# Kernel tuning notes

Measured on AMD Instinct MI355X. Metric: run time of the kernel, lower is better.

The kernel has to match this reference:

```python
import jax, jax.numpy as jnp
import numpy as np
import math

# Hardcoded model constants (from source globals)
N_LAYERS = 4
MAX_SEQ_LEN = 34
VOCAB_SIZE = 14
TOK_DIM = 3
POS_DIM = 3
D_MODEL = 6
HEAD_DIM = 3
N_POS = 10
MAX_DIGITS = 10
ANSWER_LEN = 11
X_START, PLUS_POS, Y_START, EQ_POS, Z_START, EOS_POS = 0, 10, 11, 21, 22, 33
PLUS_TOKEN, EQUALS_TOKEN, EOS_TOKEN, PAD_TOKEN = 10, 11, 12, 13
BATCH = 16384


def _spiral(i, p):
    return (math.cos(2 * math.pi * i / p), math.sin(2 * math.pi * i / p), i / max(p - 1, 1))


def _build_pos_enc():
    pe = np.zeros((MAX_SEQ_LEN, POS_DIM), np.float32)
    for i in range(MAX_DIGITS):
        pe[X_START + i] = _spiral(i, N_POS)
    for i in range(MAX_DIGITS):
        pe[Y_START + i] = _spiral(i, N_POS)
    for i in range(min(ANSWER_LEN, N_POS)):
        pe[Z_START + i] = _spiral(i, N_POS)
    pe[Z_START + 10] = [0.0, 0.0, 1.5]
    pe[PLUS_POS] = [2.0, 0.0, -1.0]
    pe[EQ_POS] = [0.0, 2.0, -1.0]
    pe[EOS_POS] = [-2.0, 0.0, -1.0]
    return jnp.asarray(pe)


def _build_tok_emb():
    emb = np.zeros((VOCAB_SIZE, TOK_DIM), np.float32)
    for d in range(10):
        emb[d] = _spiral(d, 10)
    emb[PLUS_TOKEN] = [2.0, 0.0, -1.0]
    emb[EQUALS_TOKEN] = [0.0, 2.0, -1.0]
    emb[EOS_TOKEN] = [-2.0, 0.0, -1.0]
    emb[PAD_TOKEN] = [0.0, -2.0, -1.0]
    return jnp.asarray(emb)


def _xavier(key, shape):
    fan_out, fan_in = shape[-2], shape[-1]
    bound = math.sqrt(6.0 / (fan_in + fan_out))
    return jax.random.uniform(key, shape, jnp.float32, -bound, bound)


def setup_inputs() -> dict:
    key = jax.random.key(0)
    ks = jax.random.split(key, 10)
    L = N_LAYERS
    return {
        "idx": jax.random.randint(ks[0], (BATCH, MAX_SEQ_LEN), 0, VOCAB_SIZE),
        "tok_emb": _build_tok_emb(),
        "pos_enc": _build_pos_enc(),
        "ln_w": jnp.ones((L, D_MODEL), jnp.float32),
        "ln_b": jnp.zeros((L, D_MODEL), jnp.float32),
        "q1w": _xavier(ks[1], (L, HEAD_DIM, TOK_DIM)),
        "k1w": _xavier(ks[2], (L, HEAD_DIM, TOK_DIM)),
        "v1w": _xavier(ks[3], (L, HEAD_DIM, TOK_DIM)),
        "q2w": _xavier(ks[4], (L, HEAD_DIM, POS_DIM)),
        "k2w": _xavier(ks[5], (L, HEAD_DIM, POS_DIM)),
        "v2w": _xavier(ks[6], (L, HEAD_DIM, POS_DIM)),
        "out_w": _xavier(ks[7], (L, D_MODEL, 2 * HEAD_DIM)),
        "lnf_w": jnp.ones((D_MODEL,), jnp.float32),
        "lnf_b": jnp.zeros((D_MODEL,), jnp.float32),
        "head_w": _xavier(ks[8], (VOCAB_SIZE, D_MODEL)),
    }


def _layernorm(x, w, b, eps=1e-5):
    m = jnp.mean(x, -1, keepdims=True)
    v = jnp.mean(jnp.square(x - m), -1, keepdims=True)
    return (x - m) * jax.lax.rsqrt(v + eps) * w + b


def _attend(q, k, v, mask):
    # q,k,v: [B,T,HEAD_DIM]; mask: [T,T] bool lower-triangular
    s = jnp.einsum('bqd,bkd->bqk', q, k) / math.sqrt(HEAD_DIM)
    s = jnp.where(mask, s, jnp.finfo(s.dtype).min)
    return jnp.einsum('bqk,bkd->bqd', jax.nn.softmax(s, axis=-1), v)


def reference(idx, tok_emb, pos_enc, ln_w, ln_b, q1w, k1w, v1w, q2w, k2w, v2w, out_w, lnf_w, lnf_b, head_w):
    B, T = idx.shape
    tok = tok_emb[idx]                                   # [B,T,3]
    pos = jnp.broadcast_to(pos_enc[:T], (B, T, POS_DIM))  # [B,T,3]
    x = jnp.concatenate([tok, pos], axis=-1)             # [B,T,6]
    mask = jnp.tril(jnp.ones((T, T), bool))
    for l in range(N_LAYERS):
        h = _layernorm(x, ln_w[l], ln_b[l])
        ht, hp = h[..., :TOK_DIM], h[..., TOK_DIM:]
        o1 = _attend(ht @ q1w[l].T, ht @ k1w[l].T, ht @ v1w[l].T, mask)
        o2 = _attend(hp @ q2w[l].T, hp @ k2w[l].T, hp @ v2w[l].T, mask)
        x = x + jnp.concatenate([o1, o2], axis=-1) @ out_w[l].T
    x = _layernorm(x, lnf_w, lnf_b)
    return x @ head_w.T                                  # [B,T,VOCAB]
```

## Files before the change

kernel.cpp:

```cpp
#include <hip/hip_runtime.h>
#include <math.h>

#define N_LAYERS 4
#define SEQ      34
#define BATCH_N  16384
#define NE       16
#define NSLOT    16
#define NT       3
#define VOCAB    14
#define QSCALE   0.8329806647638704f

__global__ __launch_bounds__(NE * NSLOT) void addtrans_kernel(
    const int*   __restrict__ idx,
    const float* __restrict__ tok_emb,
    const float* __restrict__ pos_enc,
    const float* __restrict__ ln_w,
    const float* __restrict__ ln_b,
    const float* __restrict__ q1w,
    const float* __restrict__ k1w,
    const float* __restrict__ v1w,
    const float* __restrict__ q2w,
    const float* __restrict__ k2w,
    const float* __restrict__ v2w,
    const float* __restrict__ out_w,
    const float* __restrict__ lnf_w,
    const float* __restrict__ lnf_b,
    const float* __restrict__ head_w,
    float* __restrict__ out)
{
    __shared__ float4 kvs[3 * SEQ + 1][NE];

    const int x = threadIdx.x & (NE - 1);
    const int y = threadIdx.x >> 4;
    const int b = (int)blockIdx.x * NE + x;

    int tp[NT];
    tp[0] = 33 - y;
    tp[1] = y;
    tp[2] = (y == 15) ? 16 : ((y == 14) ? 17 : -1);
    const int jmax = tp[0];

    float xs[NT][6];
    #pragma unroll
    for (int k = 0; k < NT; ++k) {
        const int t = tp[k];
        if (t >= 0) {
            const int tok = idx[(size_t)b * SEQ + t];
            xs[k][0] = tok_emb[tok * 3 + 0];
            xs[k][1] = tok_emb[tok * 3 + 1];
            xs[k][2] = tok_emb[tok * 3 + 2];
            xs[k][3] = pos_enc[t * 3 + 0];
            xs[k][4] = pos_enc[t * 3 + 1];
            xs[k][5] = pos_enc[t * 3 + 2];
        }
    }

    float qs[NT][6];

    for (int l = 0; l < N_LAYERS; ++l) {
        __syncthreads();

        #pragma unroll
        for (int k = 0; k < NT; ++k) {
            const int t = tp[k];
            if (t >= 0) {
                float h[6];
                {
                    const float* v = xs[k];
                    float m = (v[0]+v[1]+v[2]+v[3]+v[4]+v[5]) * (1.0f/6.0f);
                    float var = 0.f;
                    #pragma unroll
                    for (int i = 0; i < 6; ++i) { float d = v[i]-m; var += d*d; }
                    var *= (1.0f/6.0f);
                    float r = rsqrtf(var + 1e-5f);
                    #pragma unroll
                    for (int i = 0; i < 6; ++i)
                        h[i] = (v[i]-m) * r * ln_w[l*6+i] + ln_b[l*6+i];
                }
                float kk[6], vv[6];
                #pragma unroll
                for (int i = 0; i < 3; ++i) {
                    const int w = l*9 + i*3;
                    qs[k][i]   = (q1w[w]*h[0] + q1w[w+1]*h[1] + q1w[w+2]*h[2]) * QSCALE;
                    kk[i]      =  k1w[w]*h[0] + k1w[w+1]*h[1] + k1w[w+2]*h[2];
                    vv[i]      =  v1w[w]*h[0] + v1w[w+1]*h[1] + v1w[w+2]*h[2];
                    qs[k][3+i] = (q2w[w]*h[3] + q2w[w+1]*h[4] + q2w[w+2]*h[5]) * QSCALE;
                    kk[3+i]    =  k2w[w]*h[3] + k2w[w+1]*h[4] + k2w[w+2]*h[5];
                    vv[3+i]    =  v2w[w]*h[3] + v2w[w+1]*h[4] + v2w[w+2]*h[5];
                }
                kvs[0*SEQ + t][x] = make_float4(kk[0], kk[1], kk[2], kk[3]);
                kvs[1*SEQ + t][x] = make_float4(kk[4], kk[5], vv[0], vv[1]);
                kvs[2*SEQ + t][x] = make_float4(vv[2], vv[3], vv[4], vv[5]);
            }
        }
        __syncthreads();

        float l1[NT], l2[NT], a[NT][6];
        #pragma unroll
        for (int k = 0; k < NT; ++k) {
            l1[k] = 0.f; l2[k] = 0.f;
            #pragma unroll
            for (int i = 0; i < 6; ++i) a[k][i] = 0.f;
        }
        float4 c0 = kvs[0][x], c1 = kvs[SEQ][x], c2 = kvs[2*SEQ][x];
        #pragma unroll 2
        for (int j = 0; j <= jmax; ++j) {
            float4 n0 = kvs[j + 1][x];
            float4 n1 = kvs[SEQ + j + 1][x];
            float4 n2 = kvs[2*SEQ + j + 1][x];
            #pragma unroll
            for (int k = 0; k < NT; ++k) {
                if (k == 0 || j <= tp[k]) {
                    float s1 = qs[k][0]*c0.x + qs[k][1]*c0.y + qs[k][2]*c0.z;
                    float s2 = qs[k][3]*c0.w + qs[k][4]*c1.x + qs[k][5]*c1.y;
                    float p1 = __builtin_amdgcn_exp2f(s1);
                    float p2 = __builtin_amdgcn_exp2f(s2);
                    l1[k] += p1;        l2[k] += p2;
                    a[k][0] += p1*c1.z; a[k][1] += p1*c1.w; a[k][2] += p1*c2.x;
                    a[k][3] += p2*c2.y; a[k][4] += p2*c2.z; a[k][5] += p2*c2.w;
                }
            }
            c0 = n0; c1 = n1; c2 = n2;
        }

        #pragma unroll
        for (int k = 0; k < NT; ++k) {
            if (tp[k] >= 0) {
                const float i1 = __builtin_amdgcn_rcpf(l1[k]);
                const float i2 = __builtin_amdgcn_rcpf(l2[k]);
                float o[6] = { a[k][0]*i1, a[k][1]*i1, a[k][2]*i1,
                               a[k][3]*i2, a[k][4]*i2, a[k][5]*i2 };
                #pragma unroll
                for (int i = 0; i < 6; ++i) {
                    const int w = l*36 + i*6;
                    xs[k][i] += out_w[w+0]*o[0] + out_w[w+1]*o[1] + out_w[w+2]*o[2]
                              + out_w[w+3]*o[3] + out_w[w+4]*o[4] + out_w[w+5]*o[5];
                }
            }
        }
    }

    #pragma unroll
    for (int k = 0; k < NT; ++k) {
        const int t = tp[k];
        if (t >= 0) {
            float hf[6];
            {
                const float* v = xs[k];
                float m = (v[0]+v[1]+v[2]+v[3]+v[4]+v[5]) * (1.0f/6.0f);
                float var = 0.f;
                #pragma unroll
                for (int i = 0; i < 6; ++i) { float d = v[i]-m; var += d*d; }
                var *= (1.0f/6.0f);
                float r = rsqrtf(var + 1e-5f);
                #pragma unroll
                for (int i = 0; i < 6; ++i)
                    hf[i] = (v[i]-m) * r * lnf_w[i] + lnf_b[i];
            }
            float lg[VOCAB];
            #pragma unroll
            for (int c = 0; c < VOCAB; ++c) {
                const int w = c*6;
                lg[c] = head_w[w+0]*hf[0] + head_w[w+1]*hf[1] + head_w[w+2]*hf[2]
                      + head_w[w+3]*hf[3] + head_w[w+4]*hf[4] + head_w[w+5]*hf[5];
            }
            float2* op = (float2*)(out + ((size_t)b * SEQ + t) * VOCAB);
            #pragma unroll
            for (int c = 0; c < 7; ++c)
                op[c] = make_float2(lg[2*c], lg[2*c+1]);
        }
    }
}

extern "C" void kernel_launch(void* const* d_in, const int* in_sizes, int n_in,
                              void* d_out, int out_size, void* d_ws, size_t ws_size,
                              hipStream_t stream) {
    const int*   idx     = (const int*)  d_in[0];
    const float* tok_emb = (const float*)d_in[1];
    const float* pos_enc = (const float*)d_in[2];
    const float* ln_w    = (const float*)d_in[3];
    const float* ln_b    = (const float*)d_in[4];
    const float* q1w     = (const float*)d_in[5];
    const float* k1w     = (const float*)d_in[6];
    const float* v1w     = (const float*)d_in[7];
    const float* q2w     = (const float*)d_in[8];
    const float* k2w     = (const float*)d_in[9];
    const float* v2w     = (const float*)d_in[10];
    const float* out_w   = (const float*)d_in[11];
    const float* lnf_w   = (const float*)d_in[12];
    const float* lnf_b   = (const float*)d_in[13];
    const float* head_w  = (const float*)d_in[14];
    float* out = (float*)d_out;

    const int grid = BATCH_N / NE;
    addtrans_kernel<<<grid, NE * NSLOT, 0, stream>>>(
        idx, tok_emb, pos_enc, ln_w, ln_b,
        q1w, k1w, v1w, q2w, k2w, v2w,
        out_w, lnf_w, lnf_b, head_w, out);
}
```

Measured before the change: 153.1 us.

## Reassign query rows to 8 slots with strided mapping and packed float2 math

Blocks shrink from 256 to 128 threads, and each thread now owns up to five query rows spaced eight apart instead of a balanced pair of rows. The key loop is split into phases so that rows drop out as the causal range ends, which removes the per-row predicate. The two attention heads are interleaved in float2 vectors so the compiler can emit packed FP32 FMAs. The cost is more registers per thread and smaller blocks, which may reduce occupancy and change load balance across threads.

```diff
diff --git a/kernel.cpp b/kernel.cpp
--- a/kernel.cpp
+++ b/kernel.cpp
@@ -5,10 +5,16 @@
 #define SEQ      34
 #define BATCH_N  16384
 #define NE       16
-#define NSLOT    16
-#define NT       3
+#define NSLOT    8
+#define NT       5
 #define VOCAB    14
 #define QSCALE   0.8329806647638704f
+
+typedef float f32x2 __attribute__((ext_vector_type(2)));
+
+static __device__ __forceinline__ f32x2 mk2(float a, float b) {
+    f32x2 r; r.x = a; r.y = b; return r;
+}
 
 __global__ __launch_bounds__(NE * NSLOT) void addtrans_kernel(
     const int*   __restrict__ idx,
@@ -34,16 +40,17 @@
     const int y = threadIdx.x >> 4;
     const int b = (int)blockIdx.x * NE + x;
 
-    int tp[NT];
-    tp[0] = 33 - y;
-    tp[1] = y;
-    tp[2] = (y == 15) ? 16 : ((y == 14) ? 17 : -1);
-    const int jmax = tp[0];
+    int rp[NT];
+    rp[0] = y;
+    rp[1] = 8 + y;
+    rp[2] = 16 + y;
+    rp[3] = 24 + y;
+    rp[4] = (y < 2) ? (32 + y) : -1;
 
     float xs[NT][6];
     #pragma unroll
     for (int k = 0; k < NT; ++k) {
-        const int t = tp[k];
+        const int t = rp[k];
         if (t >= 0) {
             const int tok = idx[(size_t)b * SEQ + t];
             xs[k][0] = tok_emb[tok * 3 + 0];
@@ -55,14 +62,16 @@
         }
     }
 
-    float qs[NT][6];
+    f32x2 qp[NT][3];
+    #pragma unroll
+    for (int i = 0; i < 3; ++i) qp[4][i] = mk2(0.f, 0.f);
 
     for (int l = 0; l < N_LAYERS; ++l) {
         __syncthreads();
 
         #pragma unroll
         for (int k = 0; k < NT; ++k) {
-            const int t = tp[k];
+            const int t = rp[k];
             if (t >= 0) {
                 float h[6];
                 {
@@ -77,64 +86,82 @@
                     for (int i = 0; i < 6; ++i)
                         h[i] = (v[i]-m) * r * ln_w[l*6+i] + ln_b[l*6+i];
                 }
-                float kk[6], vv[6];
+                f32x2 hp0 = mk2(h[0], h[3]);
+                f32x2 hp1 = mk2(h[1], h[4]);
+                f32x2 hp2 = mk2(h[2], h[5]);
+                f32x2 kkp[3], vvp[3];
                 #pragma unroll
                 for (int i = 0; i < 3; ++i) {
                     const int w = l*9 + i*3;
-                    qs[k][i]   = (q1w[w]*h[0] + q1w[w+1]*h[1] + q1w[w+2]*h[2]) * QSCALE;
-                    kk[i]      =  k1w[w]*h[0] + k1w[w+1]*h[1] + k1w[w+2]*h[2];
-                    vv[i]      =  v1w[w]*h[0] + v1w[w+1]*h[1] + v1w[w+2]*h[2];
-                    qs[k][3+i] = (q2w[w]*h[3] + q2w[w+1]*h[4] + q2w[w+2]*h[5]) * QSCALE;
-                    kk[3+i]    =  k2w[w]*h[3] + k2w[w+1]*h[4] + k2w[w+2]*h[5];
-                    vv[3+i]    =  v2w[w]*h[3] + v2w[w+1]*h[4] + v2w[w+2]*h[5];
+                    f32x2 q = mk2(q1w[w  ], q2w[w  ]) * hp0
+                            + mk2(q1w[w+1], q2w[w+1]) * hp1
+                            + mk2(q1w[w+2], q2w[w+2]) * hp2;
+                    qp[k][i] = q * QSCALE;
+                    kkp[i]   = mk2(k1w[w  ], k2w[w  ]) * hp0
+                             + mk2(k1w[w+1], k2w[w+1]) * hp1
+                             + mk2(k1w[w+2], k2w[w+2]) * hp2;
+                    vvp[i]   = mk2(v1w[w  ], v2w[w  ]) * hp0
+                             + mk2(v1w[w+1], v2w[w+1]) * hp1
+                             + mk2(v1w[w+2], v2w[w+2]) * hp2;
                 }
-                kvs[0*SEQ + t][x] = make_float4(kk[0], kk[1], kk[2], kk[3]);
-                kvs[1*SEQ + t][x] = make_float4(kk[4], kk[5], vv[0], vv[1]);
-                kvs[2*SEQ + t][x] = make_float4(vv[2], vv[3], vv[4], vv[5]);
+                kvs[0*SEQ + t][x] = make_float4(kkp[0].x, kkp[0].y, kkp[1].x, kkp[1].y);
+                kvs[1*SEQ + t][x] = make_float4(kkp[2].x, kkp[2].y, vvp[0].x, vvp[0].y);
+                kvs[2*SEQ + t][x] = make_float4(vvp[1].x, vvp[1].y, vvp[2].x, vvp[2].y);
             }
         }
         __syncthreads();
 
-        float l1[NT], l2[NT], a[NT][6];
+        f32x2 ls[NT], acc[NT][3];
         #pragma unroll
         for (int k = 0; k < NT; ++k) {
-            l1[k] = 0.f; l2[k] = 0.f;
-            #pragma unroll
-            for (int i = 0; i < 6; ++i) a[k][i] = 0.f;
-        }
+            ls[k] = mk2(0.f, 0.f);
+            acc[k][0] = acc[k][1] = acc[k][2] = mk2(0.f, 0.f);
+        }
+
         float4 c0 = kvs[0][x], c1 = kvs[SEQ][x], c2 = kvs[2*SEQ][x];
-        #pragma unroll 2
-        for (int j = 0; j <= jmax; ++j) {
-            float4 n0 = kvs[j + 1][x];
-            float4 n1 = kvs[SEQ + j + 1][x];
-            float4 n2 = kvs[2*SEQ + j + 1][x];
-            #pragma unroll
-            for (int k = 0; k < NT; ++k) {
-                if (k == 0 || j <= tp[k]) {
-                    float s1 = qs[k][0]*c0.x + qs[k][1]*c0.y + qs[k][2]*c0.z;
-                    float s2 = qs[k][3]*c0.w + qs[k][4]*c1.x + qs[k][5]*c1.y;
-                    float p1 = __builtin_amdgcn_exp2f(s1);
-                    float p2 = __builtin_amdgcn_exp2f(s2);
-                    l1[k] += p1;        l2[k] += p2;
-                    a[k][0] += p1*c1.z; a[k][1] += p1*c1.w; a[k][2] += p1*c2.x;
-                    a[k][3] += p2*c2.y; a[k][4] += p2*c2.z; a[k][5] += p2*c2.w;
-                }
-            }
-            c0 = n0; c1 = n1; c2 = n2;
-        }
+        int j = 0;
+
+        #define LOADN \
+            float4 n0 = kvs[j + 1][x]; \
+            float4 n1 = kvs[SEQ + j + 1][x]; \
+            float4 n2 = kvs[2*SEQ + j + 1][x]; \
+            f32x2 kp0 = mk2(c0.x, c0.y), kp1 = mk2(c0.z, c0.w), kp2 = mk2(c1.x, c1.y); \
+            f32x2 vp0 = mk2(c1.z, c1.w), vp1 = mk2(c2.x, c2.y), vp2 = mk2(c2.z, c2.w);
+        #define ROWM(k) { \
+            f32x2 s = qp[k][0]*kp0 + qp[k][1]*kp1 + qp[k][2]*kp2; \
+            f32x2 p = mk2(__builtin_amdgcn_exp2f(s.x), __builtin_amdgcn_exp2f(s.y)); \
+            ls[k] += p; \
+            acc[k][0] += p*vp0; acc[k][1] += p*vp1; acc[k][2] += p*vp2; }
+        #define ROLL c0 = n0; c1 = n1; c2 = n2;
+
+        for (; j <= rp[0]; ++j) { LOADN ROWM(0) ROWM(1) ROWM(2) ROWM(3) ROWM(4) ROLL }
+        #pragma unroll
+        for (int it = 0; it < 8; ++it, ++j) { LOADN ROWM(1) ROWM(2) ROWM(3) ROWM(4) ROLL }
+        #pragma unroll
+        for (int it = 0; it < 8; ++it, ++j) { LOADN ROWM(2) ROWM(3) ROWM(4) ROLL }
+        #pragma unroll
+        for (int it = 0; it < 8; ++it, ++j) { LOADN ROWM(3) ROWM(4) ROLL }
+        for (; j <= rp[4]; ++j) { LOADN ROWM(4) ROLL }
+
+        #undef LOADN
+        #undef ROWM
+        #undef ROLL
 
         #pragma unroll
         for (int k = 0; k < NT; ++k) {
-            if (tp[k] >= 0) {
-                const float i1 = __builtin_amdgcn_rcpf(l1[k]);
-                const float i2 = __builtin_amdgcn_rcpf(l2[k]);
-                float o[6] = { a[k][0]*i1, a[k][1]*i1, a[k][2]*i1,
-                               a[k][3]*i2, a[k][4]*i2, a[k][5]*i2 };
+            if (rp[k] >= 0) {
+                const f32x2 inv = mk2(__builtin_amdgcn_rcpf(ls[k].x),
+                                      __builtin_amdgcn_rcpf(ls[k].y));
+                f32x2 op0 = acc[k][0] * inv;
+                f32x2 op1 = acc[k][1] * inv;
+                f32x2 op2 = acc[k][2] * inv;
                 #pragma unroll
                 for (int i = 0; i < 6; ++i) {
                     const int w = l*36 + i*6;
-                    xs[k][i] += out_w[w+0]*o[0] + out_w[w+1]*o[1] + out_w[w+2]*o[2]
-                              + out_w[w+3]*o[3] + out_w[w+4]*o[4] + out_w[w+5]*o[5];
+                    f32x2 t2 = mk2(out_w[w+0], out_w[w+3]) * op0
+                             + mk2(out_w[w+1], out_w[w+4]) * op1
+                             + mk2(out_w[w+2], out_w[w+5]) * op2;
+                    xs[k][i] += t2.x + t2.y;
                 }
             }
         }
@@ -142,7 +169,7 @@
 
     #pragma unroll
     for (int k = 0; k < NT; ++k) {
-        const int t = tp[k];
+        const int t = rp[k];
         if (t >= 0) {
             float hf[6];
             {
```

Result: slower. 168.9 us (+10.3%).
